# Performance work log

Measured on AMD Instinct MI355X. Metric: run time of the kernel, lower is better.

The kernel has to match this reference:

```python
import jax, jax.numpy as jnp
import numpy as np
import math

IN_C, OUT_C, KH, KW = 128, 128, 3, 3
GROUPS_NUM, NUM_W = 8, 8
STRIDE, PAD, DIL = 1, 1, 1
BETA = 1.0


def setup_inputs() -> dict:
    key = jax.random.key(0)
    ks = jax.random.split(key, 6)
    B, H, W = 8, 56, 56
    n = IN_C * KH * KW
    bound = math.sqrt(6.0 / n)  # reset_parameters bound for weight templates
    inputs = jax.random.normal(ks[0], (B, IN_C, H, W), jnp.float32)
    mask = jax.random.randint(ks[1], (B, H, W), 0, GROUPS_NUM)
    Alpha = jax.random.uniform(ks[2], (B, GROUPS_NUM, H, W), jnp.float32)
    weight_templates = jax.random.uniform(ks[3], (OUT_C * IN_C * KH * KW, NUM_W), jnp.float32, -bound, bound)
    routing_w = jax.random.normal(ks[4], (GROUPS_NUM * NUM_W, IN_C), jnp.float32) * 0.01
    routing_b = jnp.zeros((GROUPS_NUM * NUM_W,), jnp.float32)
    bias = jnp.zeros((OUT_C,), jnp.float32)
    return dict(inputs=inputs, mask=mask, Alpha=Alpha, weight_templates=weight_templates,
                routing_w=routing_w, routing_b=routing_b, bias=bias, use_alpha=1)


def _unfold(x):
    # torch F.unfold-compatible im2col: [B, C*KH*KW, Ho, Wo], channel-major feature order
    return jax.lax.conv_general_dilated_patches(
        x, (KH, KW), (STRIDE, STRIDE), [(PAD, PAD), (PAD, PAD)],
        rhs_dilation=(DIL, DIL), dimension_numbers=('NCHW', 'OIHW', 'NCHW'))


def reference(inputs, mask, Alpha, weight_templates, routing_w, routing_b, bias, use_alpha):
    B, C, H, W = inputs.shape
    K = IN_C * KH * KW
    # SE-style routing: GAP -> fc -> scaled sigmoid (alpha=1.0 in source)
    x_se = inputs.reshape(B, C, -1).mean(-1)                              # [B, C]
    x_se = 2.0 * jax.nn.sigmoid(x_se @ routing_w.T + routing_b) / NUM_W   # [B, G*num_W]
    # blend weight templates: F.linear(x_se.reshape(-1,num_W), weight)
    w = x_se.reshape(B * GROUPS_NUM, NUM_W) @ weight_templates.T          # [B*G, O*K]
    w = w.reshape(B, GROUPS_NUM, OUT_C, K).transpose(0, 2, 3, 1)          # [B, O, K, G]
    patches = _unfold(inputs)                                             # [B, K, Ho, Wo]
    # per-group convolution outputs, then per-pixel group routing
    y = jnp.einsum('bokg,bkhw->boghw', w, patches)                        # [B, O, G, Ho, Wo]
    if use_alpha:
        probs = jax.nn.softmax(BETA * Alpha, axis=1)                      # soft routing [B, G, Ho, Wo]
    else:
        probs = jax.nn.one_hot(mask, GROUPS_NUM, axis=1, dtype=y.dtype)   # hard per-pixel group select
    out = jnp.einsum('boghw,bghw->bohw', y, probs)
    return out + bias.reshape(1, -1, 1, 1)
```

## Files before the change

### kernel.cpp

```cpp
#include <hip/hip_runtime.h>
#include <stdint.h>

#define IN_C   128
#define OUT_C  128
#define KTOT   1152
#define NG     8
#define NW     8
#define NB     8
#define HH     56
#define WWID   56
#define NPIX   3136
#define PPAD   3200
#define MTOT   1024
#define HALO   58
#define HPIX   (HALO*HALO)


typedef __attribute__((ext_vector_type(8))) short short8;
typedef __attribute__((ext_vector_type(8))) unsigned short ushort8;
typedef __attribute__((ext_vector_type(4))) float f32x4;

__device__ __forceinline__ unsigned short f2bf(float f) {
    unsigned u = __float_as_uint(f);
    u += 0x7FFF + ((u >> 16) & 1);
    return (unsigned short)(u >> 16);
}

__device__ __forceinline__ void cp16(const unsigned short* g, unsigned short* l) {
    __builtin_amdgcn_global_load_lds(
        (const __attribute__((address_space(1))) unsigned int*)g,
        (__attribute__((address_space(3))) unsigned int*)l,
        16, 0, 0);
}

__global__ __launch_bounds__(256) void prep_kernel(const float* __restrict__ in,
                                                   const float* __restrict__ T,
                                                   float* __restrict__ xse,
                                                   unsigned short* __restrict__ Apack,
                                                   unsigned short* __restrict__ Xt) {
    __shared__ __align__(16) unsigned char smem[36864];
    const int blk = blockIdx.x;
    const int t = threadIdx.x;

    if (blk < 1024) {
        const float* src = in + (size_t)blk * NPIX;
        float s = 0.f;
        for (int i = t; i < NPIX / 4; i += 256) {
            float4 v = ((const float4*)src)[i];
            s += v.x + v.y + v.z + v.w;
        }
        #pragma unroll
        for (int off = 32; off; off >>= 1) s += __shfl_down(s, off);
        float* ws4 = (float*)smem;
        if ((t & 63) == 0) ws4[t >> 6] = s;
        __syncthreads();
        if (t == 0)
            xse[blk] = (ws4[0] + ws4[1] + ws4[2] + ws4[3]) * (1.0f / (float)NPIX);
        return;
    }
    if (blk < 1152) {
        float* lf = (float*)smem;
        const int o = blk - 1024;
        const float* To = T + (size_t)o * 9216;
        #pragma unroll
        for (int it = 0; it < 9; it++) {
            const int f = it * 256 + t;
            const float4 v = ((const float4*)To)[f];
            *(float4*)&lf[f * 4] = v;
        }
        __syncthreads();
        const int m16b = o >> 1;
        const int lrb = (o & 1) * 8;
        #pragma unroll
        for (int it = 0; it < 5; it++) {
            const int ch = it * 256 + t;
            if (ch < 1152) {
                const int j = ch & 7, kc = ch >> 3;
                const int s = kc >> 4, c0 = (kc & 15) << 3;
                const int kt = kc >> 2, lq = kc & 3;
                ushort8 v;
                #pragma unroll
                for (int i = 0; i < 8; i++)
                    v[i] = f2bf(lf[((c0 + i) * 9 + s) * 8 + j]);
                const size_t off = ((((size_t)m16b * 36 + kt) * 4 + lq) * 16 + lrb + j) * 8;
                *(ushort8*)&Apack[off] = v;
            }
        }
        return;
    }
    unsigned short* tile = (unsigned short*)smem;
    const int idx = blk - 1152;
    const int yt = idx % 28;
    const int b  = idx / 28;
    const int y0 = yt * 2;

    #pragma unroll
    for (int it = 0; it < 14; it++) {
        const int f = it * 256 + t;
        const int c = f / 28;
        const int rem = f - c * 28;
        const int y = rem / 14;
        const int x4 = rem - y * 14;
        const float4 v = *(const float4*)(in + ((size_t)(b * IN_C + c)) * NPIX
                                          + (y0 + y) * WWID + x4 * 4);
        unsigned short bf0 = f2bf(v.x), bf1 = f2bf(v.y), bf2 = f2bf(v.z), bf3 = f2bf(v.w);
        const int ppb = (y * WWID + x4 * 4) ^ (((c >> 3) & 15) << 2);
        uint2 pk;
        pk.x = (unsigned)bf0 | ((unsigned)bf1 << 16);
        pk.y = (unsigned)bf2 | ((unsigned)bf3 << 16);
        *(uint2*)&tile[c * 128 + ppb] = pk;
    }
    __syncthreads();

    #pragma unroll
    for (int it = 0; it < 7; it++) {
        const int ch = it * 256 + t;
        const int oct = ch & 15;
        const int pp = ch >> 4;
        const int sw = oct << 2;
        ushort8 v;
        #pragma unroll
        for (int i = 0; i < 8; i++)
            v[i] = tile[(oct * 8 + i) * 128 + (pp ^ sw)];
        const int y2 = (pp >= WWID) ? 1 : 0;
        const int xg = pp - y2 * WWID;
        const size_t hp = (size_t)b * HPIX + (y0 + y2 + 1) * HALO + (xg + 1);
        *(ushort8*)&Xt[hp * 128 + oct * 8] = v;
    }

    if (t < 64) {
        const int pi = t >> 4, oct = t & 15;
        const int yy = y0 + 1 + (pi >> 1);
        const int xx = (pi & 1) * 57;
        *(ushort8*)&Xt[((size_t)b * HPIX + yy * HALO + xx) * 128 + oct * 8] =
            (ushort8){0, 0, 0, 0, 0, 0, 0, 0};
    }
    if (yt == 0 || yt == 27) {
        const int yy = (yt == 0) ? 0 : 57;
        #pragma unroll
        for (int it = 0; it < 4; it++) {
            const int ch = it * 256 + t;
            if (ch < 928) {
                const int xx = ch >> 4, oct = ch & 15;
                *(ushort8*)&Xt[((size_t)b * HPIX + yy * HALO + xx) * 128 + oct * 8] =
                    (ushort8){0, 0, 0, 0, 0, 0, 0, 0};
            }
        }
    }
}

__global__ __launch_bounds__(256) void s_kernel(const float* __restrict__ Alpha,
                                                const int* __restrict__ mask,
                                                const float* __restrict__ xse,
                                                const float* __restrict__ rw,
                                                const float* __restrict__ rb,
                                                const int* __restrict__ use_alpha,
                                                float* __restrict__ Sws) {
    const int b = blockIdx.y;
    const int t = threadIdx.x;
    const int p = blockIdx.x * 256 + t;
    __shared__ float xs[IN_C];
    __shared__ float rsh[64];
    if (t < IN_C) xs[t] = xse[b * IN_C + t];
    __syncthreads();
    if (t < 64) {
        float acc = rb[t];
        #pragma unroll 8
        for (int c = 0; c < IN_C; c++) acc += xs[c] * rw[t * IN_C + c];
        rsh[t] = 0.25f / (1.0f + expf(-acc));
    }
    __syncthreads();
    if (p >= PPAD) return;
    float sj[8] = {0, 0, 0, 0, 0, 0, 0, 0};
    if (p < NPIX) {
        float pr[8];
        if (use_alpha[0]) {
            float a[8], m = -1e30f;
            #pragma unroll
            for (int g = 0; g < 8; g++) {
                a[g] = Alpha[((size_t)(b * NG + g)) * NPIX + p];
                m = fmaxf(m, a[g]);
            }
            float sum = 0.f;
            #pragma unroll
            for (int g = 0; g < 8; g++) { pr[g] = expf(a[g] - m); sum += pr[g]; }
            float inv = 1.f / sum;
            #pragma unroll
            for (int g = 0; g < 8; g++) pr[g] *= inv;
        } else {
            int mg = mask[(size_t)b * NPIX + p];
            #pragma unroll
            for (int g = 0; g < 8; g++) pr[g] = (g == mg) ? 1.f : 0.f;
        }
        #pragma unroll
        for (int g = 0; g < 8; g++)
            #pragma unroll
            for (int j = 0; j < 8; j++) sj[j] += pr[g] * rsh[g * 8 + j];
    }
    float* dst = Sws + ((size_t)b * PPAD + p) * 8;
    *(f32x4*)dst = (f32x4){sj[0], sj[1], sj[2], sj[3]};
    *(f32x4*)(dst + 4) = (f32x4){sj[4], sj[5], sj[6], sj[7]};
}

__global__ __launch_bounds__(256) void gemm_kernel(const unsigned short* __restrict__ Apack,
                                                   const unsigned short* __restrict__ Xt,
                                                   const float* __restrict__ Sws,
                                                   const float* __restrict__ bias,
                                                   float* __restrict__ out) {
    __shared__ __align__(16) unsigned short Bsh[2][512 * 8];
    const int tid = threadIdx.x;
    const int wv = tid >> 6, ln = tid & 63;
    const int lq = ln >> 4, lr = ln & 15;
    const int wrow = wv >> 1, wcol = wv & 1;

    const int lid = blockIdx.x;
    const int b   = lid & 7;
    const int sl  = lid >> 3;
    const int mt  = sl & 7;
    const int nt  = sl >> 3;

    f32x4 acc[4][4];
    #pragma unroll
    for (int i = 0; i < 4; i++)
        #pragma unroll
        for (int j = 0; j < 4; j++) acc[i][j] = (f32x4){0.f, 0.f, 0.f, 0.f};

    const int js = tid & 3;
    const int r0 = tid >> 2,  q0 = js ^ (r0 & 3) ^ ((r0 >> 2) & 3);
    const int r1 = r0 + 64,   q1 = js ^ (r1 & 3) ^ ((r1 >> 2) & 3);
    const int p0 = min(nt * 128 + r0, NPIX - 1);
    const int p1 = min(nt * 128 + r1, NPIX - 1);
    const int y0p = p0 / WWID, x0p = p0 - y0p * WWID;
    const int y1p = p1 / WWID, x1p = p1 - y1p * WWID;
    const unsigned short* gb0 = Xt + ((size_t)b * HPIX + y0p * HALO + x0p) * 128 + q0 * 8;
    const unsigned short* gb1 = Xt + ((size_t)b * HPIX + y1p * HALO + x1p) * 128 + q1 * 8;
    unsigned short* lb0[2] = { &Bsh[0][(wv * 64) * 8],       &Bsh[1][(wv * 64) * 8] };
    unsigned short* lb1[2] = { &Bsh[0][(256 + wv * 64) * 8], &Bsh[1][(256 + wv * 64) * 8] };

    const unsigned short* gaw[4];
    #pragma unroll
    for (int tm = 0; tm < 4; tm++) {
        const int m16 = mt * 8 + wrow * 4 + tm;
        gaw[tm] = Apack + ((size_t)m16 * 36 * 64 + ln) * 8;
    }

    const int jj = lq ^ (lr & 3) ^ ((lr >> 2) & 3);

    cp16(gb0, lb0[0]); cp16(gb1, lb1[0]);
    short8 afA[4], afB[4];
    #pragma unroll
    for (int tm = 0; tm < 4; tm++) afA[tm] = *(const short8*)(gaw[tm]);

    #pragma unroll 1
    for (int it = 0; it < 18; it++) {
        const int kk = it * 64;
        __syncthreads();
        {
            const int nk = kk + 32;
            const int s  = nk >> 7;
            const int kh = s / 3, kw = s - 3 * kh;
            const int offB = (kh * HALO + kw) * 128 + (nk & 127);
            cp16(gb0 + offB, lb0[1]); cp16(gb1 + offB, lb1[1]);
            #pragma unroll
            for (int tm = 0; tm < 4; tm++)
                afB[tm] = *(const short8*)(gaw[tm] + (size_t)(nk >> 5) * 512);
        }
        {
            short8 bfr[4];
            #pragma unroll
            for (int tn = 0; tn < 4; tn++) {
                const int row = wcol * 64 + tn * 16 + lr;
                bfr[tn] = *(const short8*)&Bsh[0][(row * 4 + jj) * 8];
            }
            #pragma unroll
            for (int tm = 0; tm < 4; tm++)
                #pragma unroll
                for (int tn = 0; tn < 4; tn++)
                    acc[tm][tn] = __builtin_amdgcn_mfma_f32_16x16x32_bf16(
                        afA[tm], bfr[tn], acc[tm][tn], 0, 0, 0);
        }
        __syncthreads();
        {
            const int nk = kk + 64;
            if (nk < KTOT) {
                const int s  = nk >> 7;
                const int kh = s / 3, kw = s - 3 * kh;
                const int offB = (kh * HALO + kw) * 128 + (nk & 127);
                cp16(gb0 + offB, lb0[0]); cp16(gb1 + offB, lb1[0]);
                #pragma unroll
                for (int tm = 0; tm < 4; tm++)
                    afA[tm] = *(const short8*)(gaw[tm] + (size_t)(nk >> 5) * 512);
            }
        }
        {
            short8 bfr[4];
            #pragma unroll
            for (int tn = 0; tn < 4; tn++) {
                const int row = wcol * 64 + tn * 16 + lr;
                bfr[tn] = *(const short8*)&Bsh[1][(row * 4 + jj) * 8];
            }
            #pragma unroll
            for (int tm = 0; tm < 4; tm++)
                #pragma unroll
                for (int tn = 0; tn < 4; tn++)
                    acc[tm][tn] = __builtin_amdgcn_mfma_f32_16x16x32_bf16(
                        afB[tm], bfr[tn], acc[tm][tn], 0, 0, 0);
        }
    }

    const int j0 = (lq & 1) * 4;
    const int oo = lq >> 1;
    #pragma unroll
    for (int tm = 0; tm < 4; tm++) {
        const int o = mt * 16 + wrow * 8 + tm * 2 + oo;
        const float bo = bias[o];
        #pragma unroll
        for (int tn = 0; tn < 4; tn++) {
            const int p = nt * 128 + wcol * 64 + tn * 16 + lr;
            const f32x4 sv = *(const f32x4*)&Sws[((size_t)b * PPAD + p) * 8 + j0];
            const f32x4 a = acc[tm][tn];
            float part = a.x * sv.x + a.y * sv.y + a.z * sv.z + a.w * sv.w;
            float tot = part + __shfl_xor(part, 16);
            if ((lq & 1) == 0 && p < NPIX)
                out[((size_t)b * OUT_C + o) * NPIX + p] = tot + bo;
        }
    }
}

extern "C" void kernel_launch(void* const* d_in, const int* in_sizes, int n_in,
                              void* d_out, int out_size, void* d_ws, size_t ws_size,
                              hipStream_t stream) {
    const float* inputs = (const float*)d_in[0];
    const int*   mask   = (const int*)d_in[1];
    const float* Alpha  = (const float*)d_in[2];
    const float* wtmpl  = (const float*)d_in[3];
    const float* rw     = (const float*)d_in[4];
    const float* rb     = (const float*)d_in[5];
    const float* bias   = (const float*)d_in[6];
    const int*   ua     = (const int*)d_in[7];
    float* out = (float*)d_out;

    char* ws = (char*)d_ws;
    unsigned short* Xt  = (unsigned short*)ws;
    unsigned short* Apk = (unsigned short*)(ws + 6889472);
    float*          Sws = (float*)(ws + 9248768);
    float*          xse = (float*)(ws + 10067968);

    prep_kernel<<<1376, 256, 0, stream>>>(inputs, wtmpl, xse, Apk, Xt);
    s_kernel<<<dim3(13, NB), 256, 0, stream>>>(Alpha, mask, xse, rw, rb, ua, Sws);
    gemm_kernel<<<1600, 256, 0, stream>>>(Apk, Xt, Sws, bias, out);
}
```

Before: 167.8 us.

## Fuse routing/softmax scale kernel into GEMM and widen K stage to 64

Removes the separate s_kernel: each GEMM block now recomputes the routing sigmoid and per-pixel softmax-weighted template scales into shared memory, eliminating a launch and the Sws global round trip. The B-tile pipeline is also restructured to load a full 64-wide K slice per stage (double-buffered, 1024 rows) with one barrier per stage instead of two, and the loop is fully unrolled. The cost is redundant routing FC work in every block (1600 blocks each do a 64x128 dot), more LDS per block, possibly lower occupancy, and more registers from full unrolling.

```diff
diff --git a/kernel.cpp b/kernel.cpp
--- a/kernel.cpp
+++ b/kernel.cpp
@@ -10,7 +10,6 @@
 #define HH     56
 #define WWID   56
 #define NPIX   3136
-#define PPAD   3200
 #define MTOT   1024
 #define HALO   58
 #define HPIX   (HALO*HALO)
@@ -149,65 +148,21 @@
     }
 }
 
-__global__ __launch_bounds__(256) void s_kernel(const float* __restrict__ Alpha,
-                                                const int* __restrict__ mask,
-                                                const float* __restrict__ xse,
-                                                const float* __restrict__ rw,
-                                                const float* __restrict__ rb,
-                                                const int* __restrict__ use_alpha,
-                                                float* __restrict__ Sws) {
-    const int b = blockIdx.y;
-    const int t = threadIdx.x;
-    const int p = blockIdx.x * 256 + t;
+__global__ __launch_bounds__(256) void gemm_kernel(const unsigned short* __restrict__ Apack,
+                                                   const unsigned short* __restrict__ Xt,
+                                                   const float* __restrict__ xse,
+                                                   const float* __restrict__ rw,
+                                                   const float* __restrict__ rb,
+                                                   const float* __restrict__ Alpha,
+                                                   const int* __restrict__ mask,
+                                                   const int* __restrict__ use_alpha,
+                                                   const float* __restrict__ bias,
+                                                   float* __restrict__ out) {
+    __shared__ __align__(16) unsigned short Bsh[2][1024 * 8];
+    __shared__ float ssh[128 * 8];
     __shared__ float xs[IN_C];
     __shared__ float rsh[64];
-    if (t < IN_C) xs[t] = xse[b * IN_C + t];
-    __syncthreads();
-    if (t < 64) {
-        float acc = rb[t];
-        #pragma unroll 8
-        for (int c = 0; c < IN_C; c++) acc += xs[c] * rw[t * IN_C + c];
-        rsh[t] = 0.25f / (1.0f + expf(-acc));
-    }
-    __syncthreads();
-    if (p >= PPAD) return;
-    float sj[8] = {0, 0, 0, 0, 0, 0, 0, 0};
-    if (p < NPIX) {
-        float pr[8];
-        if (use_alpha[0]) {
-            float a[8], m = -1e30f;
-            #pragma unroll
-            for (int g = 0; g < 8; g++) {
-                a[g] = Alpha[((size_t)(b * NG + g)) * NPIX + p];
-                m = fmaxf(m, a[g]);
-            }
-            float sum = 0.f;
-            #pragma unroll
-            for (int g = 0; g < 8; g++) { pr[g] = expf(a[g] - m); sum += pr[g]; }
-            float inv = 1.f / sum;
-            #pragma unroll
-            for (int g = 0; g < 8; g++) pr[g] *= inv;
-        } else {
-            int mg = mask[(size_t)b * NPIX + p];
-            #pragma unroll
-            for (int g = 0; g < 8; g++) pr[g] = (g == mg) ? 1.f : 0.f;
-        }
-        #pragma unroll
-        for (int g = 0; g < 8; g++)
-            #pragma unroll
-            for (int j = 0; j < 8; j++) sj[j] += pr[g] * rsh[g * 8 + j];
-    }
-    float* dst = Sws + ((size_t)b * PPAD + p) * 8;
-    *(f32x4*)dst = (f32x4){sj[0], sj[1], sj[2], sj[3]};
-    *(f32x4*)(dst + 4) = (f32x4){sj[4], sj[5], sj[6], sj[7]};
-}
-
-__global__ __launch_bounds__(256) void gemm_kernel(const unsigned short* __restrict__ Apack,
-                                                   const unsigned short* __restrict__ Xt,
-                                                   const float* __restrict__ Sws,
-                                                   const float* __restrict__ bias,
-                                                   float* __restrict__ out) {
-    __shared__ __align__(16) unsigned short Bsh[2][512 * 8];
+
     const int tid = threadIdx.x;
     const int wv = tid >> 6, ln = tid & 63;
     const int lq = ln >> 4, lr = ln & 15;
@@ -219,23 +174,15 @@
     const int mt  = sl & 7;
     const int nt  = sl >> 3;
 
-    f32x4 acc[4][4];
-    #pragma unroll
-    for (int i = 0; i < 4; i++)
-        #pragma unroll
-        for (int j = 0; j < 4; j++) acc[i][j] = (f32x4){0.f, 0.f, 0.f, 0.f};
-
-    const int js = tid & 3;
-    const int r0 = tid >> 2,  q0 = js ^ (r0 & 3) ^ ((r0 >> 2) & 3);
-    const int r1 = r0 + 64,   q1 = js ^ (r1 & 3) ^ ((r1 >> 2) & 3);
-    const int p0 = min(nt * 128 + r0, NPIX - 1);
-    const int p1 = min(nt * 128 + r1, NPIX - 1);
-    const int y0p = p0 / WWID, x0p = p0 - y0p * WWID;
-    const int y1p = p1 / WWID, x1p = p1 - y1p * WWID;
-    const unsigned short* gb0 = Xt + ((size_t)b * HPIX + y0p * HALO + x0p) * 128 + q0 * 8;
-    const unsigned short* gb1 = Xt + ((size_t)b * HPIX + y1p * HALO + x1p) * 128 + q1 * 8;
-    unsigned short* lb0[2] = { &Bsh[0][(wv * 64) * 8],       &Bsh[1][(wv * 64) * 8] };
-    unsigned short* lb1[2] = { &Bsh[0][(256 + wv * 64) * 8], &Bsh[1][(256 + wv * 64) * 8] };
+    const unsigned short* gbp[4];
+    #pragma unroll
+    for (int i = 0; i < 4; i++) {
+        const int r = i * 32 + (tid >> 3);
+        const int q = (tid & 7) ^ (r & 3) ^ ((r >> 2) & 3);
+        const int p = min(nt * 128 + r, NPIX - 1);
+        const int py = p / WWID, px = p - py * WWID;
+        gbp[i] = Xt + ((size_t)b * HPIX + py * HALO + px) * 128 + q * 8;
+    }
 
     const unsigned short* gaw[4];
     #pragma unroll
@@ -244,33 +191,84 @@
         gaw[tm] = Apack + ((size_t)m16 * 36 * 64 + ln) * 8;
     }
 
-    const int jj = lq ^ (lr & 3) ^ ((lr >> 2) & 3);
-
-    cp16(gb0, lb0[0]); cp16(gb1, lb1[0]);
+    if (tid < IN_C) xs[tid] = xse[b * IN_C + tid];
+    __syncthreads();
+    if (tid < 64) {
+        float acc = rb[tid];
+        #pragma unroll 8
+        for (int c = 0; c < IN_C; c++) acc += xs[c] * rw[tid * IN_C + c];
+        rsh[tid] = 0.25f / (1.0f + expf(-acc));
+    }
+    __syncthreads();
+
+    #pragma unroll
+    for (int i = 0; i < 4; i++) cp16(gbp[i], &Bsh[0][(i * 256 + wv * 64) * 8]);
     short8 afA[4], afB[4];
     #pragma unroll
     for (int tm = 0; tm < 4; tm++) afA[tm] = *(const short8*)(gaw[tm]);
 
-    #pragma unroll 1
-    for (int it = 0; it < 18; it++) {
-        const int kk = it * 64;
+    if (tid < 128) {
+        const int p = nt * 128 + tid;
+        float sj[8] = {0, 0, 0, 0, 0, 0, 0, 0};
+        if (p < NPIX) {
+            if (use_alpha[0]) {
+                float a[8], m = -1e30f;
+                #pragma unroll
+                for (int g = 0; g < 8; g++) {
+                    a[g] = Alpha[((size_t)(b * NG + g)) * NPIX + p];
+                    m = fmaxf(m, a[g]);
+                }
+                float pr[8], sum = 0.f;
+                #pragma unroll
+                for (int g = 0; g < 8; g++) { pr[g] = expf(a[g] - m); sum += pr[g]; }
+                const float inv = 1.f / sum;
+                #pragma unroll
+                for (int g = 0; g < 8; g++) {
+                    const float w = pr[g] * inv;
+                    #pragma unroll
+                    for (int j = 0; j < 8; j++) sj[j] += w * rsh[g * 8 + j];
+                }
+            } else {
+                const int mg = mask[(size_t)b * NPIX + p];
+                #pragma unroll
+                for (int j = 0; j < 8; j++) sj[j] = rsh[mg * 8 + j];
+            }
+        }
+        #pragma unroll
+        for (int j = 0; j < 8; j++) ssh[tid * 8 + j] = sj[j];
+    }
+
+    f32x4 acc[4][4];
+    #pragma unroll
+    for (int i = 0; i < 4; i++)
+        #pragma unroll
+        for (int j = 0; j < 4; j++) acc[i][j] = (f32x4){0.f, 0.f, 0.f, 0.f};
+
+    const int jx = lq ^ (lr & 3) ^ ((lr >> 2) & 3);
+
+    #pragma unroll
+    for (int st = 0; st < 18; st++) {
+        const int kk = st * 64;
+        const int bufc = st & 1;
         __syncthreads();
-        {
-            const int nk = kk + 32;
+        if (st + 1 < 18) {
+            const int nk = kk + 64;
             const int s  = nk >> 7;
             const int kh = s / 3, kw = s - 3 * kh;
             const int offB = (kh * HALO + kw) * 128 + (nk & 127);
-            cp16(gb0 + offB, lb0[1]); cp16(gb1 + offB, lb1[1]);
-            #pragma unroll
-            for (int tm = 0; tm < 4; tm++)
-                afB[tm] = *(const short8*)(gaw[tm] + (size_t)(nk >> 5) * 512);
-        }
+            #pragma unroll
+            for (int i = 0; i < 4; i++)
+                cp16(gbp[i] + offB, &Bsh[bufc ^ 1][(i * 256 + wv * 64) * 8]);
+        }
+        #pragma unroll
+        for (int tm = 0; tm < 4; tm++)
+            afB[tm] = *(const short8*)(gaw[tm] + (size_t)((kk + 32) >> 5) * 512);
         {
             short8 bfr[4];
             #pragma unroll
             for (int tn = 0; tn < 4; tn++) {
                 const int row = wcol * 64 + tn * 16 + lr;
-                bfr[tn] = *(const short8*)&Bsh[0][(row * 4 + jj) * 8];
+                bfr[tn] = *(const short8*)&Bsh[bufc][(row * 8 + jx) * 8];
             }
             #pragma unroll
             for (int tm = 0; tm < 4; tm++)
@@ -279,25 +277,17 @@
                     acc[tm][tn] = __builtin_amdgcn_mfma_f32_16x16x32_bf16(
                         afA[tm], bfr[tn], acc[tm][tn], 0, 0, 0);
         }
-        __syncthreads();
-        {
-            const int nk = kk + 64;
-            if (nk < KTOT) {
-                const int s  = nk >> 7;
-                const int kh = s / 3, kw = s - 3 * kh;
-                const int offB = (kh * HALO + kw) * 128 + (nk & 127);
-                cp16(gb0 + offB, lb0[0]); cp16(gb1 + offB, lb1[0]);
-                #pragma unroll
-                for (int tm = 0; tm < 4; tm++)
-                    afA[tm] = *(const short8*)(gaw[tm] + (size_t)(nk >> 5) * 512);
-            }
+        if (st + 1 < 18) {
+            #pragma unroll
+            for (int tm = 0; tm < 4; tm++)
+                afA[tm] = *(const short8*)(gaw[tm] + (size_t)((kk + 64) >> 5) * 512);
         }
         {
             short8 bfr[4];
             #pragma unroll
             for (int tn = 0; tn < 4; tn++) {
                 const int row = wcol * 64 + tn * 16 + lr;
-                bfr[tn] = *(const short8*)&Bsh[1][(row * 4 + jj) * 8];
+                bfr[tn] = *(const short8*)&Bsh[bufc][(row * 8 + 4 + jx) * 8];
             }
             #pragma unroll
             for (int tm = 0; tm < 4; tm++)
@@ -316,8 +306,9 @@
         const float bo = bias[o];
         #pragma unroll
         for (int tn = 0; tn < 4; tn++) {
-            const int p = nt * 128 + wcol * 64 + tn * 16 + lr;
-            const f32x4 sv = *(const f32x4*)&Sws[((size_t)b * PPAD + p) * 8 + j0];
+            const int pp = wcol * 64 + tn * 16 + lr;
+            const int p = nt * 128 + pp;
+            const f32x4 sv = *(const f32x4*)&ssh[pp * 8 + j0];
             const f32x4 a = acc[tm][tn];
             float part = a.x * sv.x + a.y * sv.y + a.z * sv.z + a.w * sv.w;
             float tot = part + __shfl_xor(part, 16);
@@ -343,10 +334,8 @@
     char* ws = (char*)d_ws;
     unsigned short* Xt  = (unsigned short*)ws;
     unsigned short* Apk = (unsigned short*)(ws + 6889472);
-    float*          Sws = (float*)(ws + 9248768);
-    float*          xse = (float*)(ws + 10067968);
+    float*          xse = (float*)(ws + 9248768);
 
     prep_kernel<<<1376, 256, 0, stream>>>(inputs, wtmpl, xse, Apk, Xt);
-    s_kernel<<<dim3(13, NB), 256, 0, stream>>>(Alpha, mask, xse, rw, rb, ua, Sws);
-    gemm_kernel<<<1600, 256, 0, stream>>>(Apk, Xt, Sws, bias, out);
-}
+    gemm_kernel<<<1600, 256, 0, stream>>>(Apk, Xt, xse, rw, rb, Alpha, mask, ua, bias, out);
+}
```

Measured after the change: 171.2 us. 2.0% more time.

## Deepen GEMM B-tile pipeline to four LDS buffers with one barrier per step

Applied to the files above, without the earlier changes.

The GEMM main loop moves from a two-buffer scheme with two barriers per 64-wide K step to four LDS buffers. Each step now prefetches the next two 32-wide K stages while computing on the current pair, so it needs only one __syncthreads and loads run further ahead. Separately, the weight-pack path converts templates to bf16 before staging them in LDS, which halves that shared memory. In exchange, LDS per GEMM block doubles, which could lower occupancy.

```diff
diff --git a/kernel.cpp b/kernel.cpp
--- a/kernel.cpp
+++ b/kernel.cpp
@@ -38,7 +38,7 @@
                                                    float* __restrict__ xse,
                                                    unsigned short* __restrict__ Apack,
                                                    unsigned short* __restrict__ Xt) {
-    __shared__ __align__(16) unsigned char smem[36864];
+    __shared__ __align__(16) unsigned char smem[32768];
     const int blk = blockIdx.x;
     const int t = threadIdx.x;
 
@@ -59,14 +59,16 @@
         return;
     }
     if (blk < 1152) {
-        float* lf = (float*)smem;
+        unsigned short* lh = (unsigned short*)smem;
         const int o = blk - 1024;
         const float* To = T + (size_t)o * 9216;
         #pragma unroll
         for (int it = 0; it < 9; it++) {
             const int f = it * 256 + t;
             const float4 v = ((const float4*)To)[f];
-            *(float4*)&lf[f * 4] = v;
+            ushort4 h;
+            h.x = f2bf(v.x); h.y = f2bf(v.y); h.z = f2bf(v.z); h.w = f2bf(v.w);
+            *(ushort4*)&lh[f * 4] = h;
         }
         __syncthreads();
         const int m16b = o >> 1;
@@ -81,7 +83,7 @@
                 ushort8 v;
                 #pragma unroll
                 for (int i = 0; i < 8; i++)
-                    v[i] = f2bf(lf[((c0 + i) * 9 + s) * 8 + j]);
+                    v[i] = lh[((c0 + i) * 9 + s) * 8 + j];
                 const size_t off = ((((size_t)m16b * 36 + kt) * 4 + lq) * 16 + lrb + j) * 8;
                 *(ushort8*)&Apack[off] = v;
             }
@@ -207,7 +209,7 @@
                                                    const float* __restrict__ Sws,
                                                    const float* __restrict__ bias,
                                                    float* __restrict__ out) {
-    __shared__ __align__(16) unsigned short Bsh[2][512 * 8];
+    __shared__ __align__(16) unsigned short Bsh[4][512 * 8];
     const int tid = threadIdx.x;
     const int wv = tid >> 6, ln = tid & 63;
     const int lq = ln >> 4, lr = ln & 15;
@@ -234,8 +236,9 @@
     const int y1p = p1 / WWID, x1p = p1 - y1p * WWID;
     const unsigned short* gb0 = Xt + ((size_t)b * HPIX + y0p * HALO + x0p) * 128 + q0 * 8;
     const unsigned short* gb1 = Xt + ((size_t)b * HPIX + y1p * HALO + x1p) * 128 + q1 * 8;
-    unsigned short* lb0[2] = { &Bsh[0][(wv * 64) * 8],       &Bsh[1][(wv * 64) * 8] };
-    unsigned short* lb1[2] = { &Bsh[0][(256 + wv * 64) * 8], &Bsh[1][(256 + wv * 64) * 8] };
+    unsigned short* lbA[4];
+    #pragma unroll
+    for (int i = 0; i < 4; i++) lbA[i] = &Bsh[i][(wv * 64) * 8];
 
     const unsigned short* gaw[4];
     #pragma unroll
@@ -246,65 +249,68 @@
 
     const int jj = lq ^ (lr & 3) ^ ((lr >> 2) & 3);
 
-    cp16(gb0, lb0[0]); cp16(gb1, lb1[0]);
-    short8 afA[4], afB[4];
-    #pragma unroll
-    for (int tm = 0; tm < 4; tm++) afA[tm] = *(const short8*)(gaw[tm]);
+    cp16(gb0, lbA[0]); cp16(gb1, lbA[0] + 256 * 8);
+    cp16(gb0 + 32, lbA[1]); cp16(gb1 + 32, lbA[1] + 256 * 8);
+    short8 af[2][4];
+    #pragma unroll
+    for (int tm = 0; tm < 4; tm++) af[0][tm] = *(const short8*)(gaw[tm]);
+    #pragma unroll
+    for (int tm = 0; tm < 4; tm++) af[1][tm] = *(const short8*)(gaw[tm] + 512);
 
     #pragma unroll 1
-    for (int it = 0; it < 18; it++) {
-        const int kk = it * 64;
+    for (int pr = 0; pr < 18; pr++) {
         __syncthreads();
-        {
-            const int nk = kk + 32;
-            const int s  = nk >> 7;
-            const int kh = s / 3, kw = s - 3 * kh;
-            const int offB = (kh * HALO + kw) * 128 + (nk & 127);
-            cp16(gb0 + offB, lb0[1]); cp16(gb1 + offB, lb1[1]);
-            #pragma unroll
-            for (int tm = 0; tm < 4; tm++)
-                afB[tm] = *(const short8*)(gaw[tm] + (size_t)(nk >> 5) * 512);
-        }
+        const int st2 = pr * 2 + 2, st3 = pr * 2 + 3;
+        if (pr < 17) {
+            const int nk2 = st2 * 32, s2 = nk2 >> 7;
+            const int kh2 = s2 / 3, kw2 = s2 - 3 * kh2;
+            const int off2 = (kh2 * HALO + kw2) * 128 + (nk2 & 127);
+            const int nk3 = st3 * 32, s3 = nk3 >> 7;
+            const int kh3 = s3 / 3, kw3 = s3 - 3 * kh3;
+            const int off3 = (kh3 * HALO + kw3) * 128 + (nk3 & 127);
+            unsigned short* d2 = lbA[st2 & 3];
+            unsigned short* d3 = lbA[st3 & 3];
+            cp16(gb0 + off2, d2); cp16(gb1 + off2, d2 + 256 * 8);
+            cp16(gb0 + off3, d3); cp16(gb1 + off3, d3 + 256 * 8);
+        }
+        const int bufa = (pr & 1) * 2;
         {
             short8 bfr[4];
             #pragma unroll
             for (int tn = 0; tn < 4; tn++) {
                 const int row = wcol * 64 + tn * 16 + lr;
-                bfr[tn] = *(const short8*)&Bsh[0][(row * 4 + jj) * 8];
+                bfr[tn] = *(const short8*)&Bsh[bufa][(row * 4 + jj) * 8];
             }
             #pragma unroll
             for (int tm = 0; tm < 4; tm++)
                 #pragma unroll
                 for (int tn = 0; tn < 4; tn++)
                     acc[tm][tn] = __builtin_amdgcn_mfma_f32_16x16x32_bf16(
-                        afA[tm], bfr[tn], acc[tm][tn], 0, 0, 0);
-        }
-        __syncthreads();
-        {
-            const int nk = kk + 64;
-            if (nk < KTOT) {
-                const int s  = nk >> 7;
-                const int kh = s / 3, kw = s - 3 * kh;
-                const int offB = (kh * HALO + kw) * 128 + (nk & 127);
-                cp16(gb0 + offB, lb0[0]); cp16(gb1 + offB, lb1[0]);
-                #pragma unroll
-                for (int tm = 0; tm < 4; tm++)
-                    afA[tm] = *(const short8*)(gaw[tm] + (size_t)(nk >> 5) * 512);
-            }
+                        af[0][tm], bfr[tn], acc[tm][tn], 0, 0, 0);
+        }
+        if (pr < 17) {
+            #pragma unroll
+            for (int tm = 0; tm < 4; tm++)
+                af[0][tm] = *(const short8*)(gaw[tm] + (size_t)st2 * 512);
         }
         {
             short8 bfr[4];
             #pragma unroll
             for (int tn = 0; tn < 4; tn++) {
                 const int row = wcol * 64 + tn * 16 + lr;
-                bfr[tn] = *(const short8*)&Bsh[1][(row * 4 + jj) * 8];
+                bfr[tn] = *(const short8*)&Bsh[bufa + 1][(row * 4 + jj) * 8];
             }
             #pragma unroll
             for (int tm = 0; tm < 4; tm++)
                 #pragma unroll
                 for (int tn = 0; tn < 4; tn++)
                     acc[tm][tn] = __builtin_amdgcn_mfma_f32_16x16x32_bf16(
-                        afB[tm], bfr[tn], acc[tm][tn], 0, 0, 0);
+                        af[1][tm], bfr[tn], acc[tm][tn], 0, 0, 0);
+        }
+        if (pr < 17) {
+            #pragma unroll
+            for (int tm = 0; tm < 4; tm++)
+                af[1][tm] = *(const short8*)(gaw[tm] + (size_t)st3 * 512);
         }
     }
 
```

New measurement: 165.6 us. No clear change (-1.3%).
